# Kernel tuning notes

Measured on AMD Instinct MI355X. Metric: run time of the kernel, lower is better.

The kernel has to match this reference:

```python
import jax, jax.numpy as jnp
import numpy as np

N_U, N_I, D_IN_U, D_IN_I, D, D_QOL, B = 4096, 4096, 256, 256, 256, 4, 8192

def _w(key, shape, scale=0.05):
    return (jax.random.normal(key, shape) * scale).astype(jnp.float32)

def setup_inputs() -> dict:
    key = jax.random.key(0)
    ks = jax.random.split(key, 24)
    inp = {
        "x_u": jax.random.normal(ks[0], (N_U, D_IN_U), jnp.float32),
        "x_i": jax.random.normal(ks[1], (N_I, D_IN_I), jnp.float32),
        "social_adj": jax.random.randint(ks[2], (N_U, N_U), 0, 2, jnp.int32),
        "ui_adj": jax.random.randint(ks[3], (N_U, N_I), 0, 2, jnp.int32),
        "user_idx": jax.random.randint(ks[4], (B,), 0, N_U, jnp.int32),
        "item_idx": jax.random.randint(ks[5], (B,), 0, N_I, jnp.int32),
        "q_u": jax.random.normal(ks[6], (N_U, D_QOL), jnp.float32),
        # params (Linear stored as [in, out]; y = x @ W + b)
        "user_W": _w(ks[7], (D_IN_U, D)), "user_b": jnp.zeros((D,), jnp.float32),
        "item_W": _w(ks[8], (D_IN_I, D)), "item_b": jnp.zeros((D,), jnp.float32),
        "soc_W": _w(ks[9], (D, D)), "soc_a": _w(ks[10], (2 * D,)),
        "cnt_W": _w(ks[11], (D, D)), "cnt_a": _w(ks[12], (2 * D,)),
        "gate_W": _w(ks[13], (D_QOL, D)), "gate_b": jnp.zeros((D,), jnp.float32),
        "qproj_W": _w(ks[14], (D_QOL, D)), "qproj_b": jnp.zeros((D,), jnp.float32),
        "alpha_q": jnp.float32(0.3),
        "pred_W1": _w(ks[15], (2 * D, D)), "pred_b1": jnp.zeros((D,), jnp.float32),
        "pred_W2": _w(ks[16], (D, 1)), "pred_b2": jnp.zeros((1,), jnp.float32),
    }
    return inp

def _gat(Wh_src, Wh_dst, a, adj):
    """GAT additive attention: src rows attend over dst cols where adj!=0.
    Rows with no neighbors produce zero output (matches nan_to_num + zeroing)."""
    d = Wh_src.shape[-1]
    a1 = Wh_src @ a[:d]          # [N_src]
    a2 = Wh_dst @ a[d:]          # [N_dst]
    e = jax.nn.leaky_relu(a1[:, None] + a2[None, :], 0.2)  # [N_src, N_dst]
    mask = adj != 0
    neg_inf = jnp.float32(-jnp.inf)
    m = jnp.max(jnp.where(mask, e, neg_inf), axis=-1, keepdims=True)
    m = jnp.where(jnp.isfinite(m), m, 0.0)  # guard empty rows
    ex = jnp.where(mask, jnp.exp(e - m), 0.0)
    denom = jnp.sum(ex, axis=-1, keepdims=True)
    alpha = jnp.where(denom > 0, ex / jnp.where(denom > 0, denom, 1.0), 0.0)
    out = alpha @ Wh_dst
    return out, alpha

def reference(x_u, x_i, social_adj, ui_adj, user_idx, item_idx, q_u,
              user_W, user_b, item_W, item_b, soc_W, soc_a, cnt_W, cnt_a,
              gate_W, gate_b, qproj_W, qproj_b, alpha_q,
              pred_W1, pred_b1, pred_W2, pred_b2):
    h_u = x_u @ user_W + user_b               # [N_u, D]
    h_i = x_i @ item_W + item_b               # [N_i, D]
    # social attention (users over users)
    Wh = h_u @ soc_W
    soc_msg, alpha_s = _gat(Wh, Wh, soc_a, social_adj)
    # content attention (users over items)
    Wu = h_u @ cnt_W
    Wi = h_i @ cnt_W
    cnt_msg, alpha_c = _gat(Wu, Wi, cnt_a, ui_adj)
    h_u_out = jax.nn.elu(soc_msg + cnt_msg + h_u)
    # QoL gate
    gate = jax.nn.sigmoid(q_u @ gate_W + gate_b)
    qproj = q_u @ qproj_W + qproj_b
    h_u_out = h_u_out + alpha_q * gate * qproj
    # pair prediction (dropout inactive at eval)
    cat = jnp.concatenate([h_u_out[user_idx], h_i[item_idx]], axis=-1)  # [B, 2D]
    hid = jax.nn.relu(cat @ pred_W1 + pred_b1)
    r = (hid @ pred_W2 + pred_b2)[..., 0]
    r_hat = 1.0 + 4.0 * jax.nn.sigmoid(r)
    return r_hat, alpha_s, alpha_c
```

## Files before the change

kernel.cpp:

```cpp
#include <hip/hip_runtime.h>

typedef unsigned short u16;
typedef unsigned int u32;
typedef unsigned char u8;
typedef unsigned long long u64;
typedef float f32x4 __attribute__((ext_vector_type(4)));
typedef __bf16 bf16x8 __attribute__((ext_vector_type(8)));

#define NU 4096
#define DD 256
#define BB 8192

__device__ inline u16 f2b(float f) {
    u32 u = __builtin_bit_cast(u32, f);
    u32 r = (u + 0x7fffu + ((u >> 16) & 1u)) >> 16;
    return (u16)r;
}
__device__ inline float b2f(u16 v) { return __builtin_bit_cast(float, (u32)v << 16); }
__device__ inline float lrelu(float x) { return x > 0.f ? x : 0.2f * x; }
__device__ inline float decmax(u32 e) {
    return __builtin_bit_cast(float, (e >> 31) ? (e & 0x7fffffffu) : ~e);
}

#define BARRIER_LGKM() asm volatile("s_waitcnt lgkmcnt(0)\ns_barrier" ::: "memory")

__global__ __launch_bounds__(256) void k_pro(
    const float* __restrict__ x_u, const float* __restrict__ x_i,
    const float* __restrict__ user_W, const float* __restrict__ item_W, const float* __restrict__ pred_W1,
    const float* __restrict__ soc_W, const float* __restrict__ soc_a,
    const float* __restrict__ cnt_W, const float* __restrict__ cnt_a,
    const float* __restrict__ user_b, const float* __restrict__ item_b,
    u16* __restrict__ xu_b, u16* __restrict__ xi_b,
    u16* __restrict__ uWt, u16* __restrict__ iWt, u16* __restrict__ p1Wt,
    float* __restrict__ uvec,
    u16* __restrict__ WusT, u16* __restrict__ WicT,
    float* __restrict__ b_us, float* __restrict__ b_ic, u32* __restrict__ MhEnc) {
    __shared__ float t[64][65];
    __shared__ float sa[256];
    const int b = blockIdx.x;
    const int tid = threadIdx.x;

    if (b < 1024) {
        const float* in = (b < 512) ? x_u : x_i;
        u16* out = (b < 512) ? xu_b : xi_b;
        int i = (b & 511) * 256 + tid;
        const float4 v0 = *(const float4*)(in + (size_t)i * 8);
        const float4 v1 = *(const float4*)(in + (size_t)i * 8 + 4);
        u16 u[8] = {f2b(v0.x), f2b(v0.y), f2b(v0.z), f2b(v0.w),
                    f2b(v1.x), f2b(v1.y), f2b(v1.z), f2b(v1.w)};
        *(uint4*)(out + (size_t)i * 8) = *(uint4*)u;
    } else if (b < 1088) {
        int j = b - 1024;
        const float* in;
        u16* out;
        int R;
        if (j < 16) { in = user_W; out = uWt; R = 256; }
        else if (j < 32) { in = item_W; out = iWt; R = 256; j -= 16; }
        else { in = pred_W1; out = p1Wt; R = 512; j -= 32; }
        int rb = (j >> 2) * 64, cb = (j & 3) * 64;
        for (int k = 0; k < 16; ++k) {
            int idx = k * 256 + tid;
            int lr = idx >> 6, lc = idx & 63;
            t[lr][lc] = in[(size_t)(rb + lr) * 256 + cb + lc];
        }
        __syncthreads();
        for (int k = 0; k < 16; ++k) {
            int idx = k * 256 + tid;
            int lr = idx >> 6, lc = idx & 63;
            out[(size_t)(cb + lr) * R + rb + lc] = f2b(t[lc][lr]);
        }
    } else if (b < 1092) {
        int bb = b - 1088;
        if (bb == 0 && tid < 2) MhEnc[tid] = 0u;
        const float* W = (bb < 2) ? soc_W : cnt_W;
        const float* a = ((bb < 2) ? soc_a : cnt_a) + (bb & 1) * 256;
        int lane = tid & 63, wv = tid >> 6;
        sa[tid] = a[tid];
        __syncthreads();
        for (int rr = 0; rr < 64; ++rr) {
            int in = wv * 64 + rr;
            float4 w4 = *(const float4*)(W + (size_t)in * 256 + lane * 4);
            float acc = w4.x * sa[lane * 4] + w4.y * sa[lane * 4 + 1] + w4.z * sa[lane * 4 + 2] + w4.w * sa[lane * 4 + 3];
#pragma unroll
            for (int off = 32; off; off >>= 1) acc += __shfl_down(acc, off);
            if (lane == 0) uvec[bb * 256 + in] = acc;
        }
    } else {
        int j = b - 1092;
        int p = j >> 4;
        int tile = j & 15;
        const float* A = p ? item_W : user_W;
        const float* Bw = p ? cnt_W : soc_W;
        const float* bvec = p ? item_b : user_b;
        u16* outT = p ? WicT : WusT;
        float* outb = p ? b_ic : b_us;
        int m0 = (tile >> 2) * 64, n0 = (tile & 3) * 64;
        int m = m0 + (tid >> 4) * 4, n = n0 + (tid & 15) * 4;
        float acc[4][4];
#pragma unroll
        for (int i = 0; i < 4; ++i)
#pragma unroll
            for (int k = 0; k < 4; ++k) acc[i][k] = 0.f;
        for (int k0 = 0; k0 < 256; k0 += 4) {
            float aa[4][4], bb2[4][4];
#pragma unroll
            for (int i = 0; i < 4; ++i) {
                float4 v = *(const float4*)(A + (size_t)(m + i) * 256 + k0);
                aa[i][0] = v.x; aa[i][1] = v.y; aa[i][2] = v.z; aa[i][3] = v.w;
            }
#pragma unroll
            for (int k = 0; k < 4; ++k) {
                float4 v = *(const float4*)(Bw + (size_t)(k0 + k) * 256 + n);
                bb2[k][0] = v.x; bb2[k][1] = v.y; bb2[k][2] = v.z; bb2[k][3] = v.w;
            }
#pragma unroll
            for (int i = 0; i < 4; ++i)
#pragma unroll
                for (int k = 0; k < 4; ++k)
#pragma unroll
                    for (int jj = 0; jj < 4; ++jj) acc[i][jj] += aa[i][k] * bb2[k][jj];
        }
#pragma unroll
        for (int i = 0; i < 4; ++i)
#pragma unroll
            for (int jj = 0; jj < 4; ++jj) outT[(size_t)(n + jj) * 256 + m + i] = f2b(acc[i][jj]);
        if (tile >> 2 == 0 && tid < 64) {
            int nn = n0 + tid;
            float s = 0.f;
            for (int k = 0; k < 256; ++k) s += bvec[k] * Bw[(size_t)k * 256 + nn];
            outb[nn] = s;
        }
    }
}

__global__ __launch_bounds__(256) void k_gemm4(
    const u16* __restrict__ xu_b, const u16* __restrict__ xi_b,
    const u16* __restrict__ uWt, const u16* __restrict__ iWt,
    const u16* __restrict__ WusT, const u16* __restrict__ WicT,
    const float* __restrict__ user_b, const float* __restrict__ item_b,
    const float* __restrict__ b_us, const float* __restrict__ b_ic,
    float* __restrict__ h_u_f, float* __restrict__ h_i_f, u16* __restrict__ h_i_b,
    u16* __restrict__ WhT, u16* __restrict__ WiT) {
    const int z = blockIdx.z;
    const int M = 4096, N = 256, K = 256;
    const u16* A = (z == 0 || z == 2) ? xu_b : xi_b;
    const u16* Bt = (z == 0) ? uWt : (z == 1) ? iWt : (z == 2) ? WusT : WicT;
    const float* bias = (z == 0) ? user_b : (z == 1) ? item_b : (z == 2) ? b_us : b_ic;
    float* Cf = (z == 0) ? h_u_f : (z == 1) ? h_i_f : nullptr;
    u16* Cb = (z == 1) ? h_i_b : nullptr;
    u16* Cbt = (z == 2) ? WhT : (z == 3) ? WiT : nullptr;

    __shared__ u16 As[64 * 64];
    __shared__ u16 Bs[64 * 64];
    const int tid = threadIdx.x;
    const int lane = tid & 63, wv = tid >> 6;
    const int bm = blockIdx.x * 64, bn = blockIdx.y * 64;
    const int wm = (wv >> 1) * 32, wn = (wv & 1) * 32;
    f32x4 acc[2][2];
#pragma unroll
    for (int i = 0; i < 2; i++)
#pragma unroll
        for (int j = 0; j < 2; j++) acc[i][j] = f32x4{0.f, 0.f, 0.f, 0.f};

    char* Ab = (char*)As;
    char* Bb = (char*)Bs;
    const int r = tid >> 2;
    const int ib0 = (tid & 3) * 32;
    const int swz = (r & 7) << 4;

    for (int k0 = 0; k0 < K; k0 += 64) {
        const uint4* ga = (const uint4*)(A + (size_t)(bm + r) * K + k0 + (ib0 >> 1));
        const uint4* gb = (const uint4*)(Bt + (size_t)(bn + r) * K + k0 + (ib0 >> 1));
        uint4 va0 = ga[0], va1 = ga[1];
        uint4 vb0 = gb[0], vb1 = gb[1];
        __syncthreads();
        *(uint4*)(Ab + r * 128 + ((ib0) ^ swz)) = va0;
        *(uint4*)(Ab + r * 128 + ((ib0 + 16) ^ swz)) = va1;
        *(uint4*)(Bb + r * 128 + ((ib0) ^ swz)) = vb0;
        *(uint4*)(Bb + r * 128 + ((ib0 + 16) ^ swz)) = vb1;
        __syncthreads();
#pragma unroll
        for (int kh = 0; kh < 2; ++kh) {
            bf16x8 af[2], bfr[2];
#pragma unroll
            for (int mf = 0; mf < 2; ++mf) {
                int row = wm + mf * 16 + (lane & 15);
                int kb = kh * 64 + ((lane >> 4) << 4);
                af[mf] = *(const bf16x8*)(Ab + row * 128 + (kb ^ ((row & 7) << 4)));
            }
#pragma unroll
            for (int nf = 0; nf < 2; ++nf) {
                int row = wn + nf * 16 + (lane & 15);
                int kb = kh * 64 + ((lane >> 4) << 4);
                bfr[nf] = *(const bf16x8*)(Bb + row * 128 + (kb ^ ((row & 7) << 4)));
            }
#pragma unroll
            for (int mf = 0; mf < 2; ++mf)
#pragma unroll
                for (int nf = 0; nf < 2; ++nf)
                    acc[mf][nf] = __builtin_amdgcn_mfma_f32_16x16x32_bf16(af[mf], bfr[nf], acc[mf][nf], 0, 0, 0);
        }
    }
#pragma unroll
    for (int mf = 0; mf < 2; ++mf) {
#pragma unroll
        for (int nf = 0; nf < 2; ++nf) {
            int col = bn + wn + nf * 16 + (lane & 15);
            int row0 = bm + wm + mf * 16 + ((lane >> 4) << 2);
            float bv = bias[col];
            float v[4];
#pragma unroll
            for (int q = 0; q < 4; ++q) {
                float x = acc[mf][nf][q] + bv;
                v[q] = x;
                if (Cf) Cf[(size_t)(row0 + q) * N + col] = x;
                if (Cb) Cb[(size_t)(row0 + q) * N + col] = f2b(x);
            }
            if (Cbt) {
                uint2 p;
                p.x = (u32)f2b(v[0]) | ((u32)f2b(v[1]) << 16);
                p.y = (u32)f2b(v[2]) | ((u32)f2b(v[3]) << 16);
                *(uint2*)(Cbt + (size_t)col * M + row0) = p;
            }
        }
    }
}

__global__ __launch_bounds__(256) void k_gemv_a(const float* __restrict__ h_u, const float* __restrict__ h_i,
                                                const float* __restrict__ uvec, float* __restrict__ avec,
                                                u32* __restrict__ MhEnc) {
    int tid = threadIdx.x, lane = tid & 63, wv = tid >> 6;
    int ib = blockIdx.x * 64;
    const float* H = (wv == 3) ? h_i : h_u;
    const float* u = uvec + wv * 256;
    float4 u4 = *(const float4*)(u + lane * 4);
    float runm = -1e30f;
    for (int rr = 0; rr < 64; ++rr) {
        int row = ib + rr;
        float4 h4 = *(const float4*)(H + (size_t)row * 256 + lane * 4);
        float acc = h4.x * u4.x + h4.y * u4.y + h4.z * u4.z + h4.w * u4.w;
#pragma unroll
        for (int off = 32; off; off >>= 1) acc += __shfl_down(acc, off);
        if (lane == 0) {
            avec[wv * 4096 + row] = acc;
            runm = fmaxf(runm, acc);
        }
    }
    if (lane == 0 && (wv & 1)) {
        u32 b = __builtin_bit_cast(u32, runm);
        u32 e = (b >> 31) ? ~b : (b | 0x80000000u);
        atomicMax(&MhEnc[wv >> 1], e);
    }
}

__global__ __launch_bounds__(256) void k_scan(const int* __restrict__ adjS, const int* __restrict__ adjC,
                                              const float* __restrict__ avec, const u32* __restrict__ MhEnc,
                                              float* __restrict__ dpart, u8* __restrict__ bits) {
    int z = blockIdx.z;
    const int* adj = z ? adjC : adjS;
    const float* a1 = avec + z * 8192;
    const float* a2 = a1 + 4096;
    u8* bz = bits + (size_t)z * 2097152;
    float mhg = decmax(MhEnc[z]);
    int ib = blockIdx.x * 64, jb = blockIdx.y * 512;
    int lane = threadIdx.x & 63, wv = threadIdx.x >> 6;
    float4 A0 = *(const float4*)(a2 + jb + lane * 8);
    float4 A1 = *(const float4*)(a2 + jb + lane * 8 + 4);
    const int boff = (jb >> 3) + lane;
    for (int rr = 0; rr < 16; ++rr) {
        int row = ib + wv * 16 + rr;
        float a1r = a1[row];
        float mr = lrelu(a1r + mhg);
        const int4* p = (const int4*)(adj + (size_t)row * 4096 + jb + lane * 8);
        int4 v0 = p[0], v1 = p[1];
        u32 b = (u32)(v0.x != 0) | ((u32)(v0.y != 0) << 1) | ((u32)(v0.z != 0) << 2) | ((u32)(v0.w != 0) << 3) |
                ((u32)(v1.x != 0) << 4) | ((u32)(v1.y != 0) << 5) | ((u32)(v1.z != 0) << 6) | ((u32)(v1.w != 0) << 7);
        bz[(size_t)row * 512 + boff] = (u8)b;
        float acc = 0.f;
        acc += v0.x ? __expf(lrelu(a1r + A0.x) - mr) : 0.f;
        acc += v0.y ? __expf(lrelu(a1r + A0.y) - mr) : 0.f;
        acc += v0.z ? __expf(lrelu(a1r + A0.z) - mr) : 0.f;
        acc += v0.w ? __expf(lrelu(a1r + A0.w) - mr) : 0.f;
        acc += v1.x ? __expf(lrelu(a1r + A1.x) - mr) : 0.f;
        acc += v1.y ? __expf(lrelu(a1r + A1.y) - mr) : 0.f;
        acc += v1.z ? __expf(lrelu(a1r + A1.z) - mr) : 0.f;
        acc += v1.w ? __expf(lrelu(a1r + A1.w) - mr) : 0.f;
#pragma unroll
        for (int off = 32; off; off >>= 1) acc += __shfl_down(acc, off);
        if (lane == 0) dpart[((size_t)z * 8 + blockIdx.y) * 4096 + row] = acc;
    }
}

__global__ __launch_bounds__(512, 4) void k_flash(const u8* __restrict__ bits,
                                                  const float* __restrict__ avec, const u32* __restrict__ MhEnc,
                                                  const float* __restrict__ dpart,
                                                  const u16* __restrict__ WhT, const u16* __restrict__ WiT,
                                                  float* __restrict__ out, u16* __restrict__ msgpart) {
    const int z = blockIdx.z;
    const int ib = blockIdx.x * 64;
    const int jb0 = blockIdx.y * 1024;
    const int tid = threadIdx.x, lane = tid & 63, wv = tid >> 6;
    const u8* bz = bits + (size_t)z * 2097152;
    const float* a1 = avec + z * 8192;
    const float* a2 = a1 + 4096;
    const u16* Pt = z ? WiT : WhT;
    float* alpha = out + 8192 + (size_t)z * 16777216;

    __shared__ float a2s[1024];
    __shared__ float s_a1[64], s_mr[64], s_inv[64];
    __shared__ u16 Atile[64 * 512];
    char* Ab = (char*)Atile;

    {
        float2 v = *(const float2*)(a2 + jb0 + tid * 2);
        *(float2*)(a2s + tid * 2) = v;
        if (tid < 64) {
            float a = a1[ib + tid];
            float mhg = decmax(MhEnc[z]);
            s_a1[tid] = a;
            s_mr[tid] = lrelu(a + mhg);
            float d = 0.f;
#pragma unroll
            for (int s = 0; s < 8; ++s) d += dpart[((size_t)(z * 8 + s)) * 4096 + ib + tid];
            s_inv[tid] = d > 0.f ? 1.f / d : 0.f;
        }
    }
    __syncthreads();

    f32x4 acc[4][2];
#pragma unroll
    for (int i = 0; i < 4; i++)
#pragma unroll
        for (int j = 0; j < 2; j++) acc[i][j] = f32x4{0.f, 0.f, 0.f, 0.f};

    const u16* ptb = Pt + (size_t)(wv * 32 + (lane & 15)) * 4096 + jb0 + ((lane >> 4) << 3);

    for (int sub = 0; sub < 2; ++sub) {
        const int jb = jb0 + sub * 512;
        const int bcol = (jb >> 3) + lane;
        u8 bvv[8];
#pragma unroll
        for (int rs = 0; rs < 8; ++rs)
            bvv[rs] = bz[(size_t)(ib + rs * 8 + wv) * 512 + bcol];
        const float4 a2a = *(const float4*)(a2s + sub * 512 + lane * 8);
        const float4 a2b = *(const float4*)(a2s + sub * 512 + lane * 8 + 4);
        const float av[8] = {a2a.x, a2a.y, a2a.z, a2a.w, a2b.x, a2b.y, a2b.z, a2b.w};
#pragma unroll
        for (int rs = 0; rs < 8; ++rs) {
            const int r = rs * 8 + wv;
            const float a1r = s_a1[r], mr = s_mr[r], ivr = s_inv[r];
            const u32 byte = bvv[rs];
            float al[8];
#pragma unroll
            for (int k = 0; k < 8; ++k) {
                float e = lrelu(a1r + av[k]) - mr;
                al[k] = ((byte >> k) & 1) ? __expf(e) * ivr : 0.f;
            }
            float* ap = alpha + (size_t)(ib + r) * 4096 + jb + lane * 8;
            *(float4*)ap = float4{al[0], al[1], al[2], al[3]};
            *(float4*)(ap + 4) = float4{al[4], al[5], al[6], al[7]};
            u16 pk[8];
#pragma unroll
            for (int k = 0; k < 8; ++k) pk[k] = f2b(al[k]);
            *(uint4*)(Ab + r * 1024 + ((lane * 16) ^ ((r & 7) << 4))) = *(uint4*)pk;
        }
        BARRIER_LGKM();

        const u16* pts = ptb + sub * 512;
        bf16x8 bcur0 = *(const bf16x8*)(pts);
        bf16x8 bcur1 = *(const bf16x8*)(pts + (size_t)16 * 4096);
        for (int ks = 0; ks < 16; ++ks) {
            bf16x8 bnxt0, bnxt1;
            if (ks < 15) {
                bnxt0 = *(const bf16x8*)(pts + (ks + 1) * 32);
                bnxt1 = *(const bf16x8*)(pts + (size_t)16 * 4096 + (ks + 1) * 32);
            }
#pragma unroll
            for (int mf = 0; mf < 4; ++mf) {
                int ra = mf * 16 + (lane & 15);
                bf16x8 af = *(const bf16x8*)(Ab + ra * 1024 + ((ks * 64 + ((lane >> 4) << 4)) ^ ((ra & 7) << 4)));
                acc[mf][0] = __builtin_amdgcn_mfma_f32_16x16x32_bf16(af, bcur0, acc[mf][0], 0, 0, 0);
                acc[mf][1] = __builtin_amdgcn_mfma_f32_16x16x32_bf16(af, bcur1, acc[mf][1], 0, 0, 0);
            }
            bcur0 = bnxt0;
            bcur1 = bnxt1;
        }
        BARRIER_LGKM();
    }

    u16* mp = msgpart + ((size_t)(z * 4 + blockIdx.y) * 4096 + ib) * 256;
#pragma unroll
    for (int mf = 0; mf < 4; ++mf) {
        int r0 = mf * 16 + ((lane >> 4) << 2);
#pragma unroll
        for (int nf = 0; nf < 2; ++nf) {
            int col = wv * 32 + nf * 16 + (lane & 15);
#pragma unroll
            for (int q = 0; q < 4; ++q) mp[(size_t)(r0 + q) * 256 + col] = f2b(acc[mf][nf][q]);
        }
    }
}

__global__ __launch_bounds__(256) void k_post(const u16* __restrict__ msgpart, const float* __restrict__ h_u,
                                              const float* __restrict__ q_u,
                                              const float* __restrict__ gate_W, const float* __restrict__ gate_b,
                                              const float* __restrict__ qproj_W, const float* __restrict__ qproj_b,
                                              const float* __restrict__ alpha_q, u16* __restrict__ huo_b) {
    int i = blockIdx.x;
    int n = threadIdx.x;
    float s = 0.f;
#pragma unroll
    for (int p = 0; p < 8; ++p) s += b2f(msgpart[((size_t)p * 4096 + i) * 256 + n]);
    float v = s + h_u[(size_t)i * 256 + n];
    v = v > 0.f ? v : expm1f(v);
    float q0 = q_u[i * 4 + 0], q1 = q_u[i * 4 + 1], q2 = q_u[i * 4 + 2], q3 = q_u[i * 4 + 3];
    float g = q0 * gate_W[n] + q1 * gate_W[256 + n] + q2 * gate_W[512 + n] + q3 * gate_W[768 + n] + gate_b[n];
    g = 1.f / (1.f + __expf(-g));
    float qp = q0 * qproj_W[n] + q1 * qproj_W[256 + n] + q2 * qproj_W[512 + n] + q3 * qproj_W[768 + n] + qproj_b[n];
    float o = v + alpha_q[0] * g * qp;
    huo_b[(size_t)i * 256 + n] = f2b(o);
}

__global__ __launch_bounds__(512) void k_pred(const u16* __restrict__ huo_b, const u16* __restrict__ h_i_b,
                                              const int* __restrict__ uidx, const int* __restrict__ iidx,
                                              const u16* __restrict__ Bt, const float* __restrict__ b1,
                                              const float* __restrict__ W2, const float* __restrict__ b2,
                                              float* __restrict__ out) {
    __shared__ u16 As[64 * 512];
    __shared__ float redL[512];
    const int tid = threadIdx.x, lane = tid & 63, wv = tid >> 6;
    const int bm = blockIdx.x * 64;
    char* Ab = (char*)As;

    {
        const int r = tid >> 3;
        const int uix = uidx[bm + r], iix = iidx[bm + r];
        const int sswz = (r & 7) << 4;
#pragma unroll
        for (int c = 0; c < 8; ++c) {
            int e = c * 64 + (tid & 7) * 8;
            const u16* src = (e < 256) ? (huo_b + (size_t)uix * 256 + e) : (h_i_b + (size_t)iix * 256 + (e - 256));
            uint4 v = *(const uint4*)src;
            *(uint4*)(Ab + r * 1024 + ((e * 2) ^ sswz)) = v;
        }
    }
    __syncthreads();

    const int n0 = wv * 32;
    f32x4 acc[4][2];
#pragma unroll
    for (int i = 0; i < 4; i++)
#pragma unroll
        for (int j = 0; j < 2; j++) acc[i][j] = f32x4{0.f, 0.f, 0.f, 0.f};

    for (int ks = 0; ks < 16; ++ks) {
        bf16x8 bfr[2];
#pragma unroll
        for (int nf = 0; nf < 2; ++nf)
            bfr[nf] = *(const bf16x8*)(Bt + (size_t)(n0 + nf * 16 + (lane & 15)) * 512 + ks * 32 + ((lane >> 4) << 3));
#pragma unroll
        for (int mf = 0; mf < 4; ++mf) {
            int ra = mf * 16 + (lane & 15);
            bf16x8 af = *(const bf16x8*)(Ab + ra * 1024 + ((ks * 64 + ((lane >> 4) << 4)) ^ ((ra & 7) << 4)));
#pragma unroll
            for (int nf = 0; nf < 2; ++nf)
                acc[mf][nf] = __builtin_amdgcn_mfma_f32_16x16x32_bf16(af, bfr[nf], acc[mf][nf], 0, 0, 0);
        }
    }

    float b1v[2], w2v[2];
#pragma unroll
    for (int nf = 0; nf < 2; ++nf) {
        int col = n0 + nf * 16 + (lane & 15);
        b1v[nf] = b1[col];
        w2v[nf] = W2[col];
    }
#pragma unroll
    for (int mf = 0; mf < 4; ++mf) {
#pragma unroll
        for (int q = 0; q < 4; ++q) {
            float val = 0.f;
#pragma unroll
            for (int nf = 0; nf < 2; ++nf) val += fmaxf(acc[mf][nf][q] + b1v[nf], 0.f) * w2v[nf];
#pragma unroll
            for (int off = 1; off < 16; off <<= 1) val += __shfl_xor(val, off);
            if ((lane & 15) == 0) redL[wv * 64 + mf * 16 + ((lane >> 4) << 2) + q] = val;
        }
    }
    __syncthreads();
    if (tid < 64) {
        float r = b2[0];
#pragma unroll
        for (int w = 0; w < 8; ++w) r += redL[w * 64 + tid];
        out[bm + tid] = 1.f + 4.f / (1.f + __expf(-r));
    }
}

extern "C" void kernel_launch(void* const* d_in, const int* in_sizes, int n_in,
                              void* d_out, int out_size, void* d_ws, size_t ws_size,
                              hipStream_t stream) {
    const float* x_u = (const float*)d_in[0];
    const float* x_i = (const float*)d_in[1];
    const int* adjS = (const int*)d_in[2];
    const int* adjC = (const int*)d_in[3];
    const int* uidx = (const int*)d_in[4];
    const int* iidx = (const int*)d_in[5];
    const float* q_u = (const float*)d_in[6];
    const float* user_W = (const float*)d_in[7];
    const float* user_b = (const float*)d_in[8];
    const float* item_W = (const float*)d_in[9];
    const float* item_b = (const float*)d_in[10];
    const float* soc_W = (const float*)d_in[11];
    const float* soc_a = (const float*)d_in[12];
    const float* cnt_W = (const float*)d_in[13];
    const float* cnt_a = (const float*)d_in[14];
    const float* gate_W = (const float*)d_in[15];
    const float* gate_b = (const float*)d_in[16];
    const float* qproj_W = (const float*)d_in[17];
    const float* qproj_b = (const float*)d_in[18];
    const float* alpha_q = (const float*)d_in[19];
    const float* pred_W1 = (const float*)d_in[20];
    const float* pred_b1 = (const float*)d_in[21];
    const float* pred_W2 = (const float*)d_in[22];
    const float* pred_b2 = (const float*)d_in[23];
    float* out = (float*)d_out;

    char* w = (char*)d_ws;
    size_t off = 0;
    auto alloc = [&](size_t bytes) -> void* {
        void* p = w + off;
        off = (off + bytes + 255) & ~(size_t)255;
        return p;
    };
    u16* xu_b = (u16*)alloc((size_t)NU * DD * 2);
    u16* xi_b = (u16*)alloc((size_t)NU * DD * 2);
    u16* uWt = (u16*)alloc(256 * 256 * 2);
    u16* iWt = (u16*)alloc(256 * 256 * 2);
    u16* p1Wt = (u16*)alloc(512 * 256 * 2);
    u16* WusT = (u16*)alloc(256 * 256 * 2);
    u16* WicT = (u16*)alloc(256 * 256 * 2);
    float* b_us = (float*)alloc(256 * 4);
    float* b_ic = (float*)alloc(256 * 4);
    float* uvec = (float*)alloc(4 * 256 * 4);
    float* h_u_f = (float*)alloc((size_t)NU * DD * 4);
    float* h_i_f = (float*)alloc((size_t)NU * DD * 4);
    u16* h_i_b = (u16*)alloc((size_t)NU * DD * 2);
    u16* WhT = (u16*)alloc((size_t)NU * DD * 2);
    u16* WiT = (u16*)alloc((size_t)NU * DD * 2);
    float* avec = (float*)alloc(4 * 4096 * 4);
    u32* MhEnc = (u32*)alloc(2 * 4);
    float* dpart = (float*)alloc((size_t)2 * 8 * 4096 * 4);
    u8* bits = (u8*)alloc((size_t)2 * 2097152);
    u16* msgpart = (u16*)alloc((size_t)8 * 4096 * 256 * 2);
    u16* huo_b = (u16*)alloc((size_t)NU * DD * 2);
    (void)in_sizes; (void)n_in; (void)out_size; (void)ws_size;

    k_pro<<<1124, 256, 0, stream>>>(x_u, x_i, user_W, item_W, pred_W1, soc_W, soc_a, cnt_W, cnt_a,
                                    user_b, item_b, xu_b, xi_b, uWt, iWt, p1Wt, uvec, WusT, WicT,
                                    b_us, b_ic, MhEnc);
    k_gemm4<<<dim3(64, 4, 4), 256, 0, stream>>>(xu_b, xi_b, uWt, iWt, WusT, WicT, user_b, item_b, b_us, b_ic,
                                                h_u_f, h_i_f, h_i_b, WhT, WiT);
    k_gemv_a<<<64, 256, 0, stream>>>(h_u_f, h_i_f, uvec, avec, MhEnc);
    k_scan<<<dim3(64, 8, 2), 256, 0, stream>>>(adjS, adjC, avec, MhEnc, dpart, bits);
    k_flash<<<dim3(64, 4, 2), 512, 0, stream>>>(bits, avec, MhEnc, dpart, WhT, WiT, out, msgpart);
    k_post<<<4096, 256, 0, stream>>>(msgpart, h_u_f, q_u, gate_W, gate_b, qproj_W, qproj_b, alpha_q, huo_b);
    k_pred<<<128, 512, 0, stream>>>(huo_b, h_i_b, uidx, iidx, p1Wt, pred_b1, pred_W2, pred_b2, out);
}
```

Baseline: 194.3 us.

## Fuse unnormalized PV matmul into adjacency scan, defer softmax normalization to post

The adjacency scan kernel now also builds the unnormalized exp tile in LDS and runs the MFMA product against Wh/Wi, writing per-chunk partial messages. Normalization by the row denominator moves to the post kernel, which sums 16 partials scaled by the inverse denominators. A separate lightweight kernel writes the normalized alpha matrices from the bitmask. The aim is to drop the serial dependence of the message matmul on the full denominator and cut a pass. In exchange the msgpart buffer and its traffic double, and unnormalized bf16 values can lose some precision.

```diff
diff --git a/kernel.cpp b/kernel.cpp
--- a/kernel.cpp
+++ b/kernel.cpp
@@ -253,165 +253,178 @@
     }
 }
 
-__global__ __launch_bounds__(256) void k_scan(const int* __restrict__ adjS, const int* __restrict__ adjC,
-                                              const float* __restrict__ avec, const u32* __restrict__ MhEnc,
-                                              float* __restrict__ dpart, u8* __restrict__ bits) {
-    int z = blockIdx.z;
+__global__ __launch_bounds__(512, 4) void k_scanpv(const int* __restrict__ adjS, const int* __restrict__ adjC,
+                                                   const float* __restrict__ avec, const u32* __restrict__ MhEnc,
+                                                   const u16* __restrict__ WhT, const u16* __restrict__ WiT,
+                                                   float* __restrict__ dpart, u8* __restrict__ bits,
+                                                   u16* __restrict__ msgpart) {
+    const int z = blockIdx.z;
+    const int ib = blockIdx.x * 64;
+    const int jb = blockIdx.y * 512;
+    const int tid = threadIdx.x, lane = tid & 63, wv = tid >> 6;
     const int* adj = z ? adjC : adjS;
     const float* a1 = avec + z * 8192;
     const float* a2 = a1 + 4096;
+    const u16* Pt = z ? WiT : WhT;
     u8* bz = bits + (size_t)z * 2097152;
-    float mhg = decmax(MhEnc[z]);
-    int ib = blockIdx.x * 64, jb = blockIdx.y * 512;
-    int lane = threadIdx.x & 63, wv = threadIdx.x >> 6;
-    float4 A0 = *(const float4*)(a2 + jb + lane * 8);
-    float4 A1 = *(const float4*)(a2 + jb + lane * 8 + 4);
+
+    __shared__ float a2s[512];
+    __shared__ float s_a1[64], s_mr[64];
+    __shared__ u16 Atile[64 * 512];
+    char* Ab = (char*)Atile;
+
+    if (tid < 512) a2s[tid] = a2[jb + tid];
+    if (tid < 64) {
+        float a = a1[ib + tid];
+        float mhg = decmax(MhEnc[z]);
+        s_a1[tid] = a;
+        s_mr[tid] = lrelu(a + mhg);
+    }
+    __syncthreads();
+
+    const int r0 = wv * 8;
     const int boff = (jb >> 3) + lane;
-    for (int rr = 0; rr < 16; ++rr) {
-        int row = ib + wv * 16 + rr;
-        float a1r = a1[row];
-        float mr = lrelu(a1r + mhg);
+    const float4 A0 = *(const float4*)(a2s + lane * 8);
+    const float4 A1 = *(const float4*)(a2s + lane * 8 + 4);
+    const float av[8] = {A0.x, A0.y, A0.z, A0.w, A1.x, A1.y, A1.z, A1.w};
+#pragma unroll
+    for (int rr = 0; rr < 8; ++rr) {
+        const int r = r0 + rr;
+        const int row = ib + r;
         const int4* p = (const int4*)(adj + (size_t)row * 4096 + jb + lane * 8);
         int4 v0 = p[0], v1 = p[1];
-        u32 b = (u32)(v0.x != 0) | ((u32)(v0.y != 0) << 1) | ((u32)(v0.z != 0) << 2) | ((u32)(v0.w != 0) << 3) |
-                ((u32)(v1.x != 0) << 4) | ((u32)(v1.y != 0) << 5) | ((u32)(v1.z != 0) << 6) | ((u32)(v1.w != 0) << 7);
-        bz[(size_t)row * 512 + boff] = (u8)b;
+        const float a1r = s_a1[r], mr = s_mr[r];
+        u32 bbyte = (u32)(v0.x != 0) | ((u32)(v0.y != 0) << 1) | ((u32)(v0.z != 0) << 2) | ((u32)(v0.w != 0) << 3) |
+                    ((u32)(v1.x != 0) << 4) | ((u32)(v1.y != 0) << 5) | ((u32)(v1.z != 0) << 6) | ((u32)(v1.w != 0) << 7);
+        bz[(size_t)row * 512 + boff] = (u8)bbyte;
+        float ex[8];
         float acc = 0.f;
-        acc += v0.x ? __expf(lrelu(a1r + A0.x) - mr) : 0.f;
-        acc += v0.y ? __expf(lrelu(a1r + A0.y) - mr) : 0.f;
-        acc += v0.z ? __expf(lrelu(a1r + A0.z) - mr) : 0.f;
-        acc += v0.w ? __expf(lrelu(a1r + A0.w) - mr) : 0.f;
-        acc += v1.x ? __expf(lrelu(a1r + A1.x) - mr) : 0.f;
-        acc += v1.y ? __expf(lrelu(a1r + A1.y) - mr) : 0.f;
-        acc += v1.z ? __expf(lrelu(a1r + A1.z) - mr) : 0.f;
-        acc += v1.w ? __expf(lrelu(a1r + A1.w) - mr) : 0.f;
+#pragma unroll
+        for (int k = 0; k < 8; ++k) {
+            float e = __expf(lrelu(a1r + av[k]) - mr);
+            ex[k] = ((bbyte >> k) & 1) ? e : 0.f;
+            acc += ex[k];
+        }
 #pragma unroll
         for (int off = 32; off; off >>= 1) acc += __shfl_down(acc, off);
         if (lane == 0) dpart[((size_t)z * 8 + blockIdx.y) * 4096 + row] = acc;
-    }
-}
-
-__global__ __launch_bounds__(512, 4) void k_flash(const u8* __restrict__ bits,
-                                                  const float* __restrict__ avec, const u32* __restrict__ MhEnc,
-                                                  const float* __restrict__ dpart,
-                                                  const u16* __restrict__ WhT, const u16* __restrict__ WiT,
-                                                  float* __restrict__ out, u16* __restrict__ msgpart) {
+        u16 pk[8];
+#pragma unroll
+        for (int k = 0; k < 8; ++k) pk[k] = f2b(ex[k]);
+        *(uint4*)(Ab + r * 1024 + ((lane * 16) ^ ((r & 7) << 4))) = *(uint4*)pk;
+    }
+    BARRIER_LGKM();
+
+    f32x4 acc[4][2];
+#pragma unroll
+    for (int i = 0; i < 4; i++)
+#pragma unroll
+        for (int j = 0; j < 2; j++) acc[i][j] = f32x4{0.f, 0.f, 0.f, 0.f};
+
+    const u16* pts = Pt + (size_t)(wv * 32 + (lane & 15)) * 4096 + jb + ((lane >> 4) << 3);
+    bf16x8 bcur0 = *(const bf16x8*)(pts);
+    bf16x8 bcur1 = *(const bf16x8*)(pts + (size_t)16 * 4096);
+    for (int ks = 0; ks < 16; ++ks) {
+        bf16x8 bnxt0, bnxt1;
+        if (ks < 15) {
+            bnxt0 = *(const bf16x8*)(pts + (ks + 1) * 32);
+            bnxt1 = *(const bf16x8*)(pts + (size_t)16 * 4096 + (ks + 1) * 32);
+        }
+#pragma unroll
+        for (int mf = 0; mf < 4; ++mf) {
+            int ra = mf * 16 + (lane & 15);
+            bf16x8 af = *(const bf16x8*)(Ab + ra * 1024 + ((ks * 64 + ((lane >> 4) << 4)) ^ ((ra & 7) << 4)));
+            acc[mf][0] = __builtin_amdgcn_mfma_f32_16x16x32_bf16(af, bcur0, acc[mf][0], 0, 0, 0);
+            acc[mf][1] = __builtin_amdgcn_mfma_f32_16x16x32_bf16(af, bcur1, acc[mf][1], 0, 0, 0);
+        }
+        bcur0 = bnxt0;
+        bcur1 = bnxt1;
+    }
+
+    u16* mp = msgpart + ((size_t)(z * 8 + blockIdx.y) * 4096 + ib) * 256;
+#pragma unroll
+    for (int mf = 0; mf < 4; ++mf) {
+        int rr = mf * 16 + ((lane >> 4) << 2);
+#pragma unroll
+        for (int nf = 0; nf < 2; ++nf) {
+            int col = wv * 32 + nf * 16 + (lane & 15);
+#pragma unroll
+            for (int q = 0; q < 4; ++q) mp[(size_t)(rr + q) * 256 + col] = f2b(acc[mf][nf][q]);
+        }
+    }
+}
+
+__global__ __launch_bounds__(256) void k_alpha(const u8* __restrict__ bits,
+                                               const float* __restrict__ avec, const u32* __restrict__ MhEnc,
+                                               const float* __restrict__ dpart, float* __restrict__ out) {
     const int z = blockIdx.z;
     const int ib = blockIdx.x * 64;
-    const int jb0 = blockIdx.y * 1024;
+    const int jb = blockIdx.y * 512;
     const int tid = threadIdx.x, lane = tid & 63, wv = tid >> 6;
     const u8* bz = bits + (size_t)z * 2097152;
     const float* a1 = avec + z * 8192;
     const float* a2 = a1 + 4096;
-    const u16* Pt = z ? WiT : WhT;
     float* alpha = out + 8192 + (size_t)z * 16777216;
 
-    __shared__ float a2s[1024];
     __shared__ float s_a1[64], s_mr[64], s_inv[64];
-    __shared__ u16 Atile[64 * 512];
-    char* Ab = (char*)Atile;
-
-    {
-        float2 v = *(const float2*)(a2 + jb0 + tid * 2);
-        *(float2*)(a2s + tid * 2) = v;
-        if (tid < 64) {
-            float a = a1[ib + tid];
-            float mhg = decmax(MhEnc[z]);
-            s_a1[tid] = a;
-            s_mr[tid] = lrelu(a + mhg);
-            float d = 0.f;
-#pragma unroll
-            for (int s = 0; s < 8; ++s) d += dpart[((size_t)(z * 8 + s)) * 4096 + ib + tid];
-            s_inv[tid] = d > 0.f ? 1.f / d : 0.f;
-        }
-    }
+    if (tid < 64) {
+        float a = a1[ib + tid];
+        float mhg = decmax(MhEnc[z]);
+        s_a1[tid] = a;
+        s_mr[tid] = lrelu(a + mhg);
+        float d = 0.f;
+#pragma unroll
+        for (int s = 0; s < 8; ++s) d += dpart[((size_t)(z * 8 + s)) * 4096 + ib + tid];
+        s_inv[tid] = d > 0.f ? 1.f / d : 0.f;
+    }
+    const float4 A0 = *(const float4*)(a2 + jb + lane * 4);
+    const float4 A1 = *(const float4*)(a2 + jb + 256 + lane * 4);
+    const float av0[4] = {A0.x, A0.y, A0.z, A0.w};
+    const float av1[4] = {A1.x, A1.y, A1.z, A1.w};
     __syncthreads();
 
-    f32x4 acc[4][2];
-#pragma unroll
-    for (int i = 0; i < 4; i++)
-#pragma unroll
-        for (int j = 0; j < 2; j++) acc[i][j] = f32x4{0.f, 0.f, 0.f, 0.f};
-
-    const u16* ptb = Pt + (size_t)(wv * 32 + (lane & 15)) * 4096 + jb0 + ((lane >> 4) << 3);
-
-    for (int sub = 0; sub < 2; ++sub) {
-        const int jb = jb0 + sub * 512;
-        const int bcol = (jb >> 3) + lane;
-        u8 bvv[8];
-#pragma unroll
-        for (int rs = 0; rs < 8; ++rs)
-            bvv[rs] = bz[(size_t)(ib + rs * 8 + wv) * 512 + bcol];
-        const float4 a2a = *(const float4*)(a2s + sub * 512 + lane * 8);
-        const float4 a2b = *(const float4*)(a2s + sub * 512 + lane * 8 + 4);
-        const float av[8] = {a2a.x, a2a.y, a2a.z, a2a.w, a2b.x, a2b.y, a2b.z, a2b.w};
-#pragma unroll
-        for (int rs = 0; rs < 8; ++rs) {
-            const int r = rs * 8 + wv;
-            const float a1r = s_a1[r], mr = s_mr[r], ivr = s_inv[r];
-            const u32 byte = bvv[rs];
-            float al[8];
-#pragma unroll
-            for (int k = 0; k < 8; ++k) {
-                float e = lrelu(a1r + av[k]) - mr;
-                al[k] = ((byte >> k) & 1) ? __expf(e) * ivr : 0.f;
-            }
-            float* ap = alpha + (size_t)(ib + r) * 4096 + jb + lane * 8;
-            *(float4*)ap = float4{al[0], al[1], al[2], al[3]};
-            *(float4*)(ap + 4) = float4{al[4], al[5], al[6], al[7]};
-            u16 pk[8];
-#pragma unroll
-            for (int k = 0; k < 8; ++k) pk[k] = f2b(al[k]);
-            *(uint4*)(Ab + r * 1024 + ((lane * 16) ^ ((r & 7) << 4))) = *(uint4*)pk;
-        }
-        BARRIER_LGKM();
-
-        const u16* pts = ptb + sub * 512;
-        bf16x8 bcur0 = *(const bf16x8*)(pts);
-        bf16x8 bcur1 = *(const bf16x8*)(pts + (size_t)16 * 4096);
-        for (int ks = 0; ks < 16; ++ks) {
-            bf16x8 bnxt0, bnxt1;
-            if (ks < 15) {
-                bnxt0 = *(const bf16x8*)(pts + (ks + 1) * 32);
-                bnxt1 = *(const bf16x8*)(pts + (size_t)16 * 4096 + (ks + 1) * 32);
-            }
-#pragma unroll
-            for (int mf = 0; mf < 4; ++mf) {
-                int ra = mf * 16 + (lane & 15);
-                bf16x8 af = *(const bf16x8*)(Ab + ra * 1024 + ((ks * 64 + ((lane >> 4) << 4)) ^ ((ra & 7) << 4)));
-                acc[mf][0] = __builtin_amdgcn_mfma_f32_16x16x32_bf16(af, bcur0, acc[mf][0], 0, 0, 0);
-                acc[mf][1] = __builtin_amdgcn_mfma_f32_16x16x32_bf16(af, bcur1, acc[mf][1], 0, 0, 0);
-            }
-            bcur0 = bnxt0;
-            bcur1 = bnxt1;
-        }
-        BARRIER_LGKM();
-    }
-
-    u16* mp = msgpart + ((size_t)(z * 4 + blockIdx.y) * 4096 + ib) * 256;
-#pragma unroll
-    for (int mf = 0; mf < 4; ++mf) {
-        int r0 = mf * 16 + ((lane >> 4) << 2);
-#pragma unroll
-        for (int nf = 0; nf < 2; ++nf) {
-            int col = wv * 32 + nf * 16 + (lane & 15);
-#pragma unroll
-            for (int q = 0; q < 4; ++q) mp[(size_t)(r0 + q) * 256 + col] = f2b(acc[mf][nf][q]);
-        }
-    }
-}
-
-__global__ __launch_bounds__(256) void k_post(const u16* __restrict__ msgpart, const float* __restrict__ h_u,
-                                              const float* __restrict__ q_u,
+    const int bb0 = (jb >> 3) + (lane >> 1);
+    const int sh = (lane & 1) * 4;
+    for (int rr = 0; rr < 16; ++rr) {
+        const int r = wv * 16 + rr;
+        const int row = ib + r;
+        const float a1r = s_a1[r], mr = s_mr[r], ivr = s_inv[r];
+        const u32 n0 = (u32)(bz[(size_t)row * 512 + bb0]) >> sh;
+        const u32 n1 = (u32)(bz[(size_t)row * 512 + bb0 + 32]) >> sh;
+        float o0[4], o1[4];
+#pragma unroll
+        for (int k = 0; k < 4; ++k) {
+            o0[k] = ((n0 >> k) & 1) ? __expf(lrelu(a1r + av0[k]) - mr) * ivr : 0.f;
+            o1[k] = ((n1 >> k) & 1) ? __expf(lrelu(a1r + av1[k]) - mr) * ivr : 0.f;
+        }
+        float* ap = alpha + (size_t)row * 4096 + jb;
+        *(float4*)(ap + lane * 4) = float4{o0[0], o0[1], o0[2], o0[3]};
+        *(float4*)(ap + 256 + lane * 4) = float4{o1[0], o1[1], o1[2], o1[3]};
+    }
+}
+
+__global__ __launch_bounds__(256) void k_post(const u16* __restrict__ msgpart, const float* __restrict__ dpart,
+                                              const float* __restrict__ h_u, const float* __restrict__ q_u,
                                               const float* __restrict__ gate_W, const float* __restrict__ gate_b,
                                               const float* __restrict__ qproj_W, const float* __restrict__ qproj_b,
                                               const float* __restrict__ alpha_q, u16* __restrict__ huo_b) {
     int i = blockIdx.x;
     int n = threadIdx.x;
-    float s = 0.f;
-#pragma unroll
-    for (int p = 0; p < 8; ++p) s += b2f(msgpart[((size_t)p * 4096 + i) * 256 + n]);
-    float v = s + h_u[(size_t)i * 256 + n];
+    __shared__ float red[16];
+    if (n < 16) red[n] = dpart[(size_t)n * 4096 + i];
+    __syncthreads();
+    float d0 = 0.f, d1 = 0.f;
+#pragma unroll
+    for (int p = 0; p < 8; ++p) { d0 += red[p]; d1 += red[8 + p]; }
+    float inv0 = d0 > 0.f ? 1.f / d0 : 0.f;
+    float inv1 = d1 > 0.f ? 1.f / d1 : 0.f;
+    float s0 = 0.f, s1 = 0.f;
+#pragma unroll
+    for (int p = 0; p < 8; ++p) {
+        s0 += b2f(msgpart[((size_t)p * 4096 + i) * 256 + n]);
+        s1 += b2f(msgpart[((size_t)(8 + p) * 4096 + i) * 256 + n]);
+    }
+    float v = inv0 * s0 + inv1 * s1 + h_u[(size_t)i * 256 + n];
     v = v > 0.f ? v : expm1f(v);
     float q0 = q_u[i * 4 + 0], q1 = q_u[i * 4 + 1], q2 = q_u[i * 4 + 2], q3 = q_u[i * 4 + 3];
     float g = q0 * gate_W[n] + q1 * gate_W[256 + n] + q2 * gate_W[512 + n] + q3 * gate_W[768 + n] + gate_b[n];
@@ -551,7 +564,7 @@
     u32* MhEnc = (u32*)alloc(2 * 4);
     float* dpart = (float*)alloc((size_t)2 * 8 * 4096 * 4);
     u8* bits = (u8*)alloc((size_t)2 * 2097152);
-    u16* msgpart = (u16*)alloc((size_t)8 * 4096 * 256 * 2);
+    u16* msgpart = (u16*)alloc((size_t)16 * 4096 * 256 * 2);
     u16* huo_b = (u16*)alloc((size_t)NU * DD * 2);
     (void)in_sizes; (void)n_in; (void)out_size; (void)ws_size;
 
@@ -561,8 +574,8 @@
     k_gemm4<<<dim3(64, 4, 4), 256, 0, stream>>>(xu_b, xi_b, uWt, iWt, WusT, WicT, user_b, item_b, b_us, b_ic,
                                                 h_u_f, h_i_f, h_i_b, WhT, WiT);
     k_gemv_a<<<64, 256, 0, stream>>>(h_u_f, h_i_f, uvec, avec, MhEnc);
-    k_scan<<<dim3(64, 8, 2), 256, 0, stream>>>(adjS, adjC, avec, MhEnc, dpart, bits);
-    k_flash<<<dim3(64, 4, 2), 512, 0, stream>>>(bits, avec, MhEnc, dpart, WhT, WiT, out, msgpart);
-    k_post<<<4096, 256, 0, stream>>>(msgpart, h_u_f, q_u, gate_W, gate_b, qproj_W, qproj_b, alpha_q, huo_b);
+    k_scanpv<<<dim3(64, 8, 2), 512, 0, stream>>>(adjS, adjC, avec, MhEnc, WhT, WiT, dpart, bits, msgpart);
+    k_alpha<<<dim3(64, 8, 2), 256, 0, stream>>>(bits, avec, MhEnc, dpart, out);
+    k_post<<<4096, 256, 0, stream>>>(msgpart, dpart, h_u_f, q_u, gate_W, gate_b, qproj_W, qproj_b, alpha_q, huo_b);
     k_pred<<<128, 512, 0, stream>>>(huo_b, h_i_b, uidx, iidx, p1Wt, pred_b1, pred_W2, pred_b2, out);
 }
```

After: 191.1 us. About the same (-1.6%).
